# Kernel tuning notes

Measured on AMD Instinct MI355X. Metric: run time of the kernel, lower is better.

## Reference

```python
import jax, jax.numpy as jnp
import numpy as np

B, NV, NL, D, H = 32, 512, 256, 1024, 4096


def _ffn(x, w1, b1, w2, b2):
    # torch FFN: linear2(relu(linear1(x))); weights stored as [in, out]
    return jnp.maximum(x @ w1 + b1, 0.0) @ w2 + b2


def setup_inputs() -> dict:
    key = jax.random.key(0)
    ks = jax.random.split(key, 12)
    s_in = 1.0 / np.sqrt(D)
    s_h = 1.0 / np.sqrt(H)
    return {
        "V": jax.random.normal(ks[0], (B, NV, D), jnp.float32),
        "L": jax.random.normal(ks[1], (B, NL, D), jnp.float32),
        "v_mask": jnp.ones((B, NV), jnp.float32),
        "l_mask": jnp.ones((B, NL), jnp.float32),
        "w1_V": jax.random.normal(ks[2], (D, H), jnp.float32) * s_in,
        "b1_V": jnp.zeros((H,), jnp.float32),
        "w2_V": jax.random.normal(ks[3], (H, D), jnp.float32) * s_h,
        "b2_V": jnp.zeros((D,), jnp.float32),
        "w1_L": jax.random.normal(ks[4], (D, H), jnp.float32) * s_in,
        "b1_L": jnp.zeros((H,), jnp.float32),
        "w2_L": jax.random.normal(ks[5], (H, D), jnp.float32) * s_h,
        "b2_L": jnp.zeros((D,), jnp.float32),
    }


def reference(V, L, v_mask, l_mask, w1_V, b1_V, w2_V, b2_V, w1_L, b1_L, w2_L, b2_L):
    # masks are unused in the original forward
    fV_V = _ffn(V, w1_V, b1_V, w2_V, b2_V)  # [B, NV, D] = ffn_V(V)
    fL_L = _ffn(L, w1_L, b1_L, w2_L, b2_L)  # [B, NL, D] = ffn_L(L)
    fL_V = _ffn(V, w1_L, b1_L, w2_L, b2_L)  # [B, NV, D] = ffn_L(V) (as in source)
    scale = 1.0 / jnp.sqrt(jnp.asarray(V.shape[-1], V.dtype))
    A_LV = jnp.einsum('bnd,bmd->bnm', fV_V, fL_L) * scale  # [B, NV, NL]
    A_VV = jnp.einsum('bnd,bmd->bnm', fV_V, fL_V) * scale  # [B, NV, NV]
    A = jnp.concatenate([A_LV, A_VV], axis=-1)             # [B, NV, NL+NV]
    # softmax over dim=1 (rows), as in the source
    attn = jax.nn.softmax(A, axis=1)
    KV = jnp.concatenate([fL_L, fV_V], axis=1)              # [B, NL+NV, D]
    V_next = jnp.einsum('bnk,bkd->bnd', attn, KV)           # [B, NV, D]
    return (A, V_next)
```

## Files before the change

### kernel.cpp

```cpp
#include <hip/hip_runtime.h>
#include <stdint.h>

#define B_   32
#define NV_  512
#define NL_  256
#define D_   1024
#define H_   4096
#define KTOT 768
#define SCALE_ 0.03125f

typedef __attribute__((ext_vector_type(8))) __bf16 bf8_t;
typedef __attribute__((ext_vector_type(4))) float f32x4;

__device__ __forceinline__ unsigned short f2bf(float f) {
    unsigned u = __float_as_uint(f);
    u += 0x7FFFu + ((u >> 16) & 1u);
    return (unsigned short)(u >> 16);
}
__device__ __forceinline__ unsigned pk2(float lo, float hi) {
    return (unsigned)f2bf(lo) | ((unsigned)f2bf(hi) << 16);
}

__device__ __forceinline__ void gl_lds16(const void* g, const void* lds) {
    __builtin_amdgcn_global_load_lds(
        (const __attribute__((address_space(1))) unsigned int*)(uintptr_t)g,
        (__attribute__((address_space(3))) unsigned int*)(unsigned)(uintptr_t)lds,
        16, 0, 0);
}

#define SBAR() asm volatile("s_barrier" ::: "memory")
#define VMC4() asm volatile("s_waitcnt vmcnt(4)" ::: "memory")
#define VMC0() asm volatile("s_waitcnt vmcnt(0)" ::: "memory")

template<int EPI>
__global__ __launch_bounds__(512, 1)
void gemm256(const unsigned short* __restrict__ Ab, long sAz, int lda,
             const unsigned short* __restrict__ Bb, long sBz, int ldb,
             const float* __restrict__ bias,
             unsigned short* __restrict__ Cp, long sCz, int ldc, int K,
             int nx, int ntile, int tpc)
{
    extern __shared__ unsigned char lds[];
    unsigned char* const ldsA = lds;
    unsigned char* const ldsB = lds + 65536;

    const int tid = threadIdx.x;
    const int w = tid >> 6, l = tid & 63;
    const int wr = w >> 2, wc = w & 3;
    const int lrow = l & 15;
    const int kg = l >> 4;

    int t_, z;
    {
        const int bid = blockIdx.x;
        if (tpc > 0) { const int r = bid >> 3, c = bid & 7; z = r / tpc; t_ = c * tpc + r % tpc; }
        else         { z = bid / ntile; t_ = bid - z * ntile; }
    }
    const int n0 = (t_ % nx) * 256, m0 = (t_ / nx) * 256;

    const unsigned short* A  = Ab + (long)z * sAz;
    const unsigned short* Bg = Bb + (long)z * sBz;

    const int srow = tid >> 3;
    const int scol = ((tid & 7) * 8) ^ ((srow & 7) << 3);
    const int ntk = K >> 6;

    const int cs0 = (((l >> 4) * 16)) ^ ((l & 7) << 4);
    const int cs1 = (64 + ((l >> 4) * 16)) ^ ((l & 7) << 4);

    const unsigned short* const sp0 = Bg + (long)(n0 +   0 + srow) * ldb + scol;
    const unsigned short* const sp1 = Bg + (long)(n0 + 128 + srow) * ldb + scol;
    const unsigned short* const sp2 = A  + (long)(m0 +   0 + srow) * lda + scol;
    const unsigned short* const sp3 = A  + (long)(m0 + 128 + srow) * lda + scol;
    const long stB = (long)64 * ldb, stA = (long)64 * lda;

    f32x4 acc[8][4];
#pragma unroll
    for (int i = 0; i < 8; ++i)
#pragma unroll
        for (int j = 0; j < 4; ++j) acc[i][j] = (f32x4){0.f, 0.f, 0.f, 0.f};

#define STG(tau, part) do {                                                   \
        const int buf_ = (tau) & 1;                                           \
        const int kt_ = ((tau) < ntk ? (tau) : ntk - 1);                      \
        if ((part) < 2) {                                                     \
            const unsigned short* s_ = ((part) == 0 ? sp0 : sp1) + (long)kt_ * 64; \
            unsigned char* d_ = ldsB + (buf_ * 2 + (part)) * 16384 + w * 1024;\
            gl_lds16(s_, d_); gl_lds16(s_ + stB, d_ + 8192);                  \
        } else {                                                              \
            const unsigned short* s_ = ((part) == 2 ? sp2 : sp3) + (long)kt_ * 64; \
            unsigned char* d_ = ldsA + (buf_ * 2 + (part) - 2) * 16384 + w * 1024; \
            gl_lds16(s_, d_); gl_lds16(s_ + stA, d_ + 8192);                  \
        } } while (0)

    auto rdA = [&](int buf, int mf, int cs) -> bf8_t {
        return *(const bf8_t*)(ldsA + (buf * 2 + wr) * 16384 + (mf * 16 + lrow) * 128 + cs);
    };
    auto rdB = [&](int buf, int nf, int cs) -> bf8_t {
        return *(const bf8_t*)(ldsB + (buf * 2 + (wc >> 1)) * 16384 +
                               ((wc & 1) * 64 + nf * 16 + lrow) * 128 + cs);
    };

#define MQ(MO, NO, AREG, BREG)                                                \
    _Pragma("unroll")                                                         \
    for (int mf = 0; mf < 4; ++mf)                                            \
    _Pragma("unroll")                                                         \
        for (int nf = 0; nf < 2; ++nf) {                                      \
            acc[(MO)+mf][(NO)+nf] = __builtin_amdgcn_mfma_f32_16x16x32_bf16(  \
                AREG[mf][0], BREG[nf][0], acc[(MO)+mf][(NO)+nf], 0, 0, 0);    \
            acc[(MO)+mf][(NO)+nf] = __builtin_amdgcn_mfma_f32_16x16x32_bf16(  \
                AREG[mf][1], BREG[nf][1], acc[(MO)+mf][(NO)+nf], 0, 0, 0);    \
        }

    STG(0, 0); STG(0, 1); STG(0, 2); STG(0, 3);
    STG(1, 0); STG(1, 1);
    VMC4();
    SBAR();

    bf8_t a0[4][2], b0r[2][2], b1r[2][2];

#define TILE4(BUF, TAU)                                                       \
                      \
    _Pragma("unroll")                                                         \
    for (int mf = 0; mf < 4; ++mf) { a0[mf][0] = rdA(BUF, mf, cs0);           \
                                     a0[mf][1] = rdA(BUF, mf, cs1); }         \
    _Pragma("unroll")                                                         \
    for (int nf = 0; nf < 2; ++nf) { b0r[nf][0] = rdB(BUF, nf, cs0);          \
                                     b0r[nf][1] = rdB(BUF, nf, cs1); }        \
    STG((TAU) + 1, 2);                                                        \
    SBAR();                                                                   \
    __builtin_amdgcn_s_setprio(1);                                            \
    _Pragma("unroll")                                                         \
    for (int nf = 0; nf < 2; ++nf) { b1r[nf][0] = rdB(BUF, nf + 2, cs0);      \
                                     b1r[nf][1] = rdB(BUF, nf + 2, cs1); }    \
    MQ(0, 0, a0, b0r)                                                         \
    __builtin_amdgcn_s_setprio(0);                                            \
    SBAR();                                                                   \
                                                                      \
    STG((TAU) + 1, 3);                                                        \
    SBAR();                                                                   \
    __builtin_amdgcn_s_setprio(1);                                            \
    MQ(0, 2, a0, b1r)                                                         \
    __builtin_amdgcn_s_setprio(0);                                            \
    SBAR();                                                                   \
                           \
    _Pragma("unroll")                                                         \
    for (int mf = 0; mf < 4; ++mf) { a0[mf][0] = rdA(BUF, mf + 4, cs0);       \
                                     a0[mf][1] = rdA(BUF, mf + 4, cs1); }     \
    STG((TAU) + 2, 0);                                                        \
    SBAR();                                                                   \
    __builtin_amdgcn_s_setprio(1);                                            \
    MQ(4, 0, a0, b0r)                                                         \
    __builtin_amdgcn_s_setprio(0);                                            \
    SBAR();                                                                   \
                                                                      \
    STG((TAU) + 2, 1);                                                        \
    SBAR();                                                                   \
    VMC4();                                                                   \
    __builtin_amdgcn_s_setprio(1);                                            \
    MQ(4, 2, a0, b1r)                                                         \
    __builtin_amdgcn_s_setprio(0);                                            \
    SBAR();

    for (int t = 0; t < ntk; t += 2) {
        TILE4(0, t)
        TILE4(1, t + 1)
    }
#undef TILE4
#undef MQ
#undef STG

    VMC0();
    SBAR();

    unsigned short* C = Cp + (long)z * sCz;
    unsigned char* const scr = lds + w * 16384;

    float bv[4];
#pragma unroll
    for (int nf = 0; nf < 4; ++nf) bv[nf] = bias[n0 + wc * 64 + nf * 16 + lrow];

#pragma unroll
    for (int p = 0; p < 2; ++p) {
#pragma unroll
        for (int mf = 0; mf < 4; ++mf)
#pragma unroll
            for (int nf = 0; nf < 4; ++nf)
#pragma unroll
                for (int r = 0; r < 4; ++r) {
                    float v = acc[4 * p + mf][nf][r] + bv[nf];
                    if (EPI == 0) v = fmaxf(v, 0.f);
                    *(unsigned short*)(scr + (mf * 16 + kg * 4 + r) * 136 +
                                       (nf * 16 + lrow) * 2) = f2bf(v);
                }
#pragma unroll
        for (int it = 0; it < 8; ++it) {
            const int rr = it * 8 + (l >> 3);
            const uint4 q = *(const uint4*)(scr + rr * 136 + (l & 7) * 16);
            *(uint4*)(C + (long)(m0 + wr * 128 + p * 64 + rr) * ldc +
                      (n0 + wc * 64 + (l & 7) * 8)) = q;
        }
    }
}

__device__ __forceinline__ void supertile(int nx, int tpc, int& n0, int& m0, int& z)
{
    const int bid = blockIdx.x;
    const int r = bid >> 3, c = bid & 7;
    z = r / tpc;
    const int t = c * tpc + (r % tpc);
    n0 = (t % nx) * 128;
    m0 = (t / nx) * 128;
}

template<int EPI>
__global__ __launch_bounds__(256)
void mgemm(const unsigned short* __restrict__ Ab, long sAz, int lda,
           const unsigned short* __restrict__ Bb, long sBz, int ldb,
           const float* __restrict__ bias, float scale,
           void* __restrict__ Cp, long sCz, int ldc, int K,
           int nx, int tpc)
{
    __shared__ unsigned short As[128 * 32];
    __shared__ unsigned short Bs[128 * 32];

    const int tid = threadIdx.x;
    const int w = tid >> 6, l = tid & 63;
    const int wr = w >> 1, wc = w & 1;
    const int l15 = l & 15, kg = l >> 4;
    const int srow = l >> 2, scol = (l & 3) * 8;
    int n0, m0, z;
    supertile(nx, tpc, n0, m0, z);

    const unsigned short* A  = Ab + (long)z * sAz;
    const unsigned short* Bg = Bb + (long)z * sBz;

    f32x4 acc[4][4];
#pragma unroll
    for (int m = 0; m < 4; ++m)
#pragma unroll
        for (int n = 0; n < 4; ++n) acc[m][n] = (f32x4){0.f, 0.f, 0.f, 0.f};

    for (int k0 = 0; k0 < K; k0 += 32) {
#pragma unroll
        for (int i = 0; i < 2; ++i) {
            const int g = i * 4 + w;
            gl_lds16(A  + (long)(m0 + g * 16 + srow) * lda + (k0 + scol), &As[g * 512]);
            gl_lds16(Bg + (long)(n0 + g * 16 + srow) * ldb + (k0 + scol), &Bs[g * 512]);
        }
        __syncthreads();

        bf8_t af[4], bf[4];
#pragma unroll
        for (int m = 0; m < 4; ++m)
            af[m] = *(const bf8_t*)&As[(wr * 64 + m * 16 + l15) * 32 + kg * 8];
#pragma unroll
        for (int n = 0; n < 4; ++n)
            bf[n] = *(const bf8_t*)&Bs[(wc * 64 + n * 16 + l15) * 32 + kg * 8];
#pragma unroll
        for (int m = 0; m < 4; ++m)
#pragma unroll
            for (int n = 0; n < 4; ++n)
                acc[m][n] = __builtin_amdgcn_mfma_f32_16x16x32_bf16(af[m], bf[n], acc[m][n], 0, 0, 0);
        __syncthreads();
    }

    const int orow = wr * 64 + (l >> 4) * 4;
    const int ocol = wc * 64 + l15;
    if (EPI == 2) {
        float* C = (float*)Cp + (long)z * sCz;
#pragma unroll
        for (int m = 0; m < 4; ++m)
#pragma unroll
            for (int n = 0; n < 4; ++n)
#pragma unroll
                for (int r = 0; r < 4; ++r)
                    C[(long)(m0 + orow + m * 16 + r) * ldc + (n0 + ocol + n * 16)] =
                        acc[m][n][r] * scale;
    } else {
        unsigned short* C = (unsigned short*)Cp + (long)z * sCz;
#pragma unroll
        for (int n = 0; n < 4; ++n) {
            const float bvv = bias[n0 + ocol + n * 16];
#pragma unroll
            for (int m = 0; m < 4; ++m)
#pragma unroll
                for (int r = 0; r < 4; ++r) {
                    float v = acc[m][n][r] + bvv;
                    if (EPI == 0) v = fmaxf(v, 0.f);
                    C[(long)(m0 + orow + m * 16 + r) * ldc + (n0 + ocol + n * 16)] = f2bf(v);
                }
        }
    }
}

__global__ __launch_bounds__(256)
void col_stats(const float* __restrict__ A, float* __restrict__ Mst, float* __restrict__ RS)
{
    __shared__ float red[4][64];
    const int t = threadIdx.x;
    const int kk = t & 63, ng = t >> 6;
    const int k = blockIdx.x * 64 + kk;
    const int z = blockIdx.y;
    const float* base = A + (long)z * NV_ * KTOT + k;
    float m = -3.0e38f;
    for (int n = ng * 128; n < ng * 128 + 128; ++n) m = fmaxf(m, base[(long)n * KTOT]);
    red[ng][kk] = m;
    __syncthreads();
    m = fmaxf(fmaxf(red[0][kk], red[1][kk]), fmaxf(red[2][kk], red[3][kk]));
    float s = 0.f;
    for (int n = ng * 128; n < ng * 128 + 128; ++n) s += __expf(base[(long)n * KTOT] - m);
    __syncthreads();
    red[ng][kk] = s;
    __syncthreads();
    if (ng == 0) {
        s = red[0][kk] + red[1][kk] + red[2][kk] + red[3][kk];
        Mst[(long)z * KTOT + k] = m;
        RS[(long)z * KTOT + k]  = 1.f / s;
    }
}

__global__ __launch_bounds__(256)
void attn_mfma(const float* __restrict__ Ap, const unsigned short* __restrict__ KVt,
               const float* __restrict__ Mstp, const float* __restrict__ RSp,
               float* __restrict__ Cp, int nx, int tpc)
{
    __shared__ unsigned short As[128 * 32];
    __shared__ unsigned short Bs[128 * 32];

    const int tid = threadIdx.x;
    const int w = tid >> 6, l = tid & 63;
    const int wr = w >> 1, wc = w & 1;
    const int l15 = l & 15, kg = l >> 4;
    const int srow = l >> 2, scol = (l & 3) * 8;
    int n0, m0, z;
    supertile(nx, tpc, n0, m0, z);

    const float* A = Ap + (long)z * NV_ * KTOT;
    const unsigned short* Bg = KVt + (long)z * D_ * KTOT;
    const float* Mz = Mstp + (long)z * KTOT;
    const float* Rz = RSp  + (long)z * KTOT;
    float* C = Cp + (long)z * NV_ * D_;

    const int ar = tid >> 1;
    const int ah = (tid & 1) * 16;

    f32x4 acc[4][4];
#pragma unroll
    for (int m = 0; m < 4; ++m)
#pragma unroll
        for (int n = 0; n < 4; ++n) acc[m][n] = (f32x4){0.f, 0.f, 0.f, 0.f};

    for (int k0 = 0; k0 < KTOT; k0 += 32) {
#pragma unroll
        for (int i = 0; i < 2; ++i) {
            const int g = i * 4 + w;
            gl_lds16(Bg + (long)(n0 + g * 16 + srow) * KTOT + (k0 + scol), &Bs[g * 512]);
        }
        const float* arow = A + (long)(m0 + ar) * KTOT + k0 + ah;
        const float4 x0 = *(const float4*)(arow);
        const float4 x1 = *(const float4*)(arow + 4);
        const float4 x2 = *(const float4*)(arow + 8);
        const float4 x3 = *(const float4*)(arow + 12);
        const float4 ma = *(const float4*)(Mz + k0 + ah);
        const float4 mb = *(const float4*)(Mz + k0 + ah + 4);
        const float4 mc = *(const float4*)(Mz + k0 + ah + 8);
        const float4 md = *(const float4*)(Mz + k0 + ah + 12);
        const float4 ra = *(const float4*)(Rz + k0 + ah);
        const float4 rb = *(const float4*)(Rz + k0 + ah + 4);
        const float4 rc = *(const float4*)(Rz + k0 + ah + 8);
        const float4 rd = *(const float4*)(Rz + k0 + ah + 12);
        const unsigned q0 = pk2(__expf(x0.x - ma.x) * ra.x, __expf(x0.y - ma.y) * ra.y);
        const unsigned q1 = pk2(__expf(x0.z - ma.z) * ra.z, __expf(x0.w - ma.w) * ra.w);
        const unsigned q2 = pk2(__expf(x1.x - mb.x) * rb.x, __expf(x1.y - mb.y) * rb.y);
        const unsigned q3 = pk2(__expf(x1.z - mb.z) * rb.z, __expf(x1.w - mb.w) * rb.w);
        const unsigned q4 = pk2(__expf(x2.x - mc.x) * rc.x, __expf(x2.y - mc.y) * rc.y);
        const unsigned q5 = pk2(__expf(x2.z - mc.z) * rc.z, __expf(x2.w - mc.w) * rc.w);
        const unsigned q6 = pk2(__expf(x3.x - md.x) * rd.x, __expf(x3.y - md.y) * rd.y);
        const unsigned q7 = pk2(__expf(x3.z - md.z) * rd.z, __expf(x3.w - md.w) * rd.w);
        *(uint4*)&As[ar * 32 + ah]     = make_uint4(q0, q1, q2, q3);
        *(uint4*)&As[ar * 32 + ah + 8] = make_uint4(q4, q5, q6, q7);
        __syncthreads();

        bf8_t af[4], bf[4];
#pragma unroll
        for (int m = 0; m < 4; ++m)
            af[m] = *(const bf8_t*)&As[(wr * 64 + m * 16 + l15) * 32 + kg * 8];
#pragma unroll
        for (int n = 0; n < 4; ++n)
            bf[n] = *(const bf8_t*)&Bs[(wc * 64 + n * 16 + l15) * 32 + kg * 8];
#pragma unroll
        for (int m = 0; m < 4; ++m)
#pragma unroll
            for (int n = 0; n < 4; ++n)
                acc[m][n] = __builtin_amdgcn_mfma_f32_16x16x32_bf16(af[m], bf[n], acc[m][n], 0, 0, 0);
        __syncthreads();
    }

    const int orow = wr * 64 + (l >> 4) * 4;
    const int ocol = wc * 64 + l15;
#pragma unroll
    for (int m = 0; m < 4; ++m)
#pragma unroll
        for (int n = 0; n < 4; ++n)
#pragma unroll
            for (int r = 0; r < 4; ++r)
                C[(long)(m0 + orow + m * 16 + r) * D_ + (n0 + ocol + n * 16)] = acc[m][n][r];
}

__global__ __launch_bounds__(256)
void tr2bf_f(const float* __restrict__ src, long sSz, int ldS,
             unsigned short* __restrict__ dst, long sDz, int ldD)
{
    __shared__ unsigned short T[64][65];
    const int t = threadIdx.x;
    const int rr = t >> 2, cc = (t & 3) * 16;
    const int r0 = blockIdx.x * 64, c0 = blockIdx.y * 64, z = blockIdx.z;
    const float* S = src + (long)z * sSz + (long)(r0 + rr) * ldS + c0 + cc;
    const float4 a = *(const float4*)(S);
    const float4 b = *(const float4*)(S + 4);
    const float4 c = *(const float4*)(S + 8);
    const float4 d = *(const float4*)(S + 12);
    unsigned short* Tr = &T[rr][cc];
    Tr[0] = f2bf(a.x); Tr[1] = f2bf(a.y); Tr[2]  = f2bf(a.z); Tr[3]  = f2bf(a.w);
    Tr[4] = f2bf(b.x); Tr[5] = f2bf(b.y); Tr[6]  = f2bf(b.z); Tr[7]  = f2bf(b.w);
    Tr[8] = f2bf(c.x); Tr[9] = f2bf(c.y); Tr[10] = f2bf(c.z); Tr[11] = f2bf(c.w);
    Tr[12] = f2bf(d.x); Tr[13] = f2bf(d.y); Tr[14] = f2bf(d.z); Tr[15] = f2bf(d.w);
    __syncthreads();
    unsigned short v[16];
#pragma unroll
    for (int j = 0; j < 16; ++j) v[j] = T[cc + j][rr];
    unsigned q[8];
#pragma unroll
    for (int j = 0; j < 8; ++j) q[j] = (unsigned)v[2 * j] | ((unsigned)v[2 * j + 1] << 16);
    unsigned short* Dp = dst + (long)z * sDz + (long)(c0 + rr) * ldD + r0 + cc;
    *(uint4*)Dp       = make_uint4(q[0], q[1], q[2], q[3]);
    *(uint4*)(Dp + 8) = make_uint4(q[4], q[5], q[6], q[7]);
}

__global__ __launch_bounds__(256)
void tr2bf_h(const unsigned short* __restrict__ src, long sSz, int ldS,
             unsigned short* __restrict__ dst, long sDz, int ldD)
{
    __shared__ unsigned short T[64][65];
    const int t = threadIdx.x;
    const int rr = t >> 2, cc = (t & 3) * 16;
    const int r0 = blockIdx.x * 64, c0 = blockIdx.y * 64, z = blockIdx.z;
    const unsigned short* S = src + (long)z * sSz + (long)(r0 + rr) * ldS + c0 + cc;
    const uint4 qa = *(const uint4*)(S);
    const uint4 qb = *(const uint4*)(S + 8);
    unsigned short* Tr = &T[rr][cc];
    Tr[0]  = qa.x & 0xFFFF; Tr[1]  = qa.x >> 16; Tr[2]  = qa.y & 0xFFFF; Tr[3]  = qa.y >> 16;
    Tr[4]  = qa.z & 0xFFFF; Tr[5]  = qa.z >> 16; Tr[6]  = qa.w & 0xFFFF; Tr[7]  = qa.w >> 16;
    Tr[8]  = qb.x & 0xFFFF; Tr[9]  = qb.x >> 16; Tr[10] = qb.y & 0xFFFF; Tr[11] = qb.y >> 16;
    Tr[12] = qb.z & 0xFFFF; Tr[13] = qb.z >> 16; Tr[14] = qb.w & 0xFFFF; Tr[15] = qb.w >> 16;
    __syncthreads();
    unsigned short v[16];
#pragma unroll
    for (int j = 0; j < 16; ++j) v[j] = T[cc + j][rr];
    unsigned q[8];
#pragma unroll
    for (int j = 0; j < 8; ++j) q[j] = (unsigned)v[2 * j] | ((unsigned)v[2 * j + 1] << 16);
    unsigned short* Dp = dst + (long)z * sDz + (long)(c0 + rr) * ldD + r0 + cc;
    *(uint4*)Dp       = make_uint4(q[0], q[1], q[2], q[3]);
    *(uint4*)(Dp + 8) = make_uint4(q[4], q[5], q[6], q[7]);
}

__global__ __launch_bounds__(256)
void cvt_bf(const float* __restrict__ src, unsigned short* __restrict__ dst, long n)
{
    const long i = ((long)blockIdx.x * 256 + threadIdx.x) * 8;
    if (i >= n) return;
    const float4 a = *(const float4*)(src + i);
    const float4 b = *(const float4*)(src + i + 4);
    *(uint4*)(dst + i) = make_uint4(pk2(a.x, a.y), pk2(a.z, a.w), pk2(b.x, b.y), pk2(b.z, b.w));
}

extern "C" void kernel_launch(void* const* d_in, const int* in_sizes, int n_in,
                              void* d_out, int out_size, void* d_ws, size_t ws_size,
                              hipStream_t stream)
{
    (void)in_sizes; (void)n_in; (void)out_size;

    const float* V   = (const float*)d_in[0];
    const float* L   = (const float*)d_in[1];
    const float* w1V = (const float*)d_in[4];
    const float* b1V = (const float*)d_in[5];
    const float* w2V = (const float*)d_in[6];
    const float* b2V = (const float*)d_in[7];
    const float* w1L = (const float*)d_in[8];
    const float* b1L = (const float*)d_in[9];
    const float* w2L = (const float*)d_in[10];
    const float* b2L = (const float*)d_in[11];

    float* outA = (float*)d_out;
    float* outV = outA + (size_t)B_ * NV_ * KTOT;

    unsigned short* w1Vt = (unsigned short*)d_ws;
    unsigned short* w2Vt = w1Vt + (size_t)H_ * D_;
    unsigned short* w1Lt = w2Vt + (size_t)D_ * H_;
    unsigned short* w2Lt = w1Lt + (size_t)H_ * D_;
    unsigned short* pool = w2Lt + (size_t)D_ * H_;

    const size_t perb_us = (size_t)NV_ * D_ + (size_t)NL_ * D_ + (size_t)NV_ * H_ +
                           (size_t)NV_ * D_ + (size_t)NL_ * D_ + (size_t)NV_ * D_ +
                           (size_t)D_ * KTOT;
    const size_t perb_bytes = perb_us * 2 + 2 * (size_t)KTOT * sizeof(float);
    const size_t persist_bytes = (size_t)4 * H_ * D_ * 2;
    const size_t avail = (ws_size > persist_bytes + 256) ? ws_size - persist_bytes - 256 : 0;
    int bc = (int)(avail / perb_bytes);
    if (bc > B_) bc = B_;
    if (bc < 1)  bc = 1;

    unsigned short* Vb  = pool;
    unsigned short* Lb  = Vb  + (size_t)bc * NV_ * D_;
    unsigned short* hid = Lb  + (size_t)bc * NL_ * D_;
    unsigned short* fV  = hid + (size_t)bc * NV_ * H_;
    unsigned short* fLL = fV  + (size_t)bc * NV_ * D_;
    unsigned short* fLV = fLL + (size_t)bc * NL_ * D_;
    unsigned short* KVt = fLV + (size_t)bc * NV_ * D_;
    float* Mst = (float*)(KVt + (size_t)bc * D_ * KTOT);
    float* RS  = Mst + (size_t)bc * KTOT;

    const dim3 blk(256);
    const dim3 blk5(512);

    {
        auto* f0 = gemm256<0>;
        auto* f1 = gemm256<1>;
        hipFuncSetAttribute((const void*)f0, hipFuncAttributeMaxDynamicSharedMemorySize, 131072);
        hipFuncSetAttribute((const void*)f1, hipFuncAttributeMaxDynamicSharedMemorySize, 131072);
    }

    tr2bf_f<<<dim3(D_ / 64, H_ / 64, 1), blk, 0, stream>>>(w1V, 0, H_, w1Vt, 0, D_);
    tr2bf_f<<<dim3(H_ / 64, D_ / 64, 1), blk, 0, stream>>>(w2V, 0, D_, w2Vt, 0, H_);
    tr2bf_f<<<dim3(D_ / 64, H_ / 64, 1), blk, 0, stream>>>(w1L, 0, H_, w1Lt, 0, D_);
    tr2bf_f<<<dim3(H_ / 64, D_ / 64, 1), blk, 0, stream>>>(w2L, 0, D_, w2Lt, 0, H_);

    for (int b0 = 0; b0 < B_; b0 += bc) {
        const int cur = (B_ - b0 < bc) ? (B_ - b0) : bc;

        cvt_bf<<<dim3(cur * NV_ * D_ / 2048), blk, 0, stream>>>(
            V + (size_t)b0 * NV_ * D_, Vb, (long)cur * NV_ * D_);
        cvt_bf<<<dim3(cur * NL_ * D_ / 2048), blk, 0, stream>>>(
            L + (size_t)b0 * NL_ * D_, Lb, (long)cur * NL_ * D_);

        #define G256(M, N) dim3((unsigned)(((N) / 256) * ((M) / 256) * cur)), blk5, 131072, stream
        #define P256(M, N) (N) / 256, (((N) / 256) * ((M) / 256)), \
                           ((((N) / 256) * ((M) / 256)) % 8 == 0 ? (((N) / 256) * ((M) / 256)) / 8 : 0)

        gemm256<0><<<G256(NV_, H_)>>>(Vb, (long)NV_ * D_, D_, w1Vt, 0, D_, b1V,
                                      hid, (long)NV_ * H_, H_, D_, P256(NV_, H_));
        gemm256<1><<<G256(NV_, D_)>>>(hid, (long)NV_ * H_, H_, w2Vt, 0, H_, b2V,
                                      fV, (long)NV_ * D_, D_, H_, P256(NV_, D_));
        gemm256<0><<<G256(NL_, H_)>>>(Lb, (long)NL_ * D_, D_, w1Lt, 0, D_, b1L,
                                      hid, (long)NV_ * H_, H_, D_, P256(NL_, H_));
        gemm256<1><<<G256(NL_, D_)>>>(hid, (long)NV_ * H_, H_, w2Lt, 0, H_, b2L,
                                      fLL, (long)NL_ * D_, D_, H_, P256(NL_, D_));
        gemm256<0><<<G256(NV_, H_)>>>(Vb, (long)NV_ * D_, D_, w1Lt, 0, D_, b1L,
                                      hid, (long)NV_ * H_, H_, D_, P256(NV_, H_));
        gemm256<1><<<G256(NV_, D_)>>>(hid, (long)NV_ * H_, H_, w2Lt, 0, H_, b2L,
                                      fLV, (long)NV_ * D_, D_, H_, P256(NV_, D_));
        #undef G256
        #undef P256

        #define GRID(nx, ny) dim3((unsigned)((nx) * (ny) * cur)), blk
        #define SWZ(nx, ny)  (nx), ((nx) * (ny) / 8)
        mgemm<2><<<GRID(NL_ / 128, NV_ / 128), 0, stream>>>(
            fV, (long)NV_ * D_, D_, fLL, (long)NL_ * D_, D_, nullptr, SCALE_,
            outA + (size_t)b0 * NV_ * KTOT, (long)NV_ * KTOT, KTOT, D_,
            SWZ(NL_ / 128, NV_ / 128));
        mgemm<2><<<GRID(NV_ / 128, NV_ / 128), 0, stream>>>(
            fV, (long)NV_ * D_, D_, fLV, (long)NV_ * D_, D_, nullptr, SCALE_,
            outA + (size_t)b0 * NV_ * KTOT + NL_, (long)NV_ * KTOT, KTOT, D_,
            SWZ(NV_ / 128, NV_ / 128));

        tr2bf_h<<<dim3(NL_ / 64, D_ / 64, cur), blk, 0, stream>>>(
            fLL, (long)NL_ * D_, D_, KVt, (long)D_ * KTOT, KTOT);
        tr2bf_h<<<dim3(NV_ / 64, D_ / 64, cur), blk, 0, stream>>>(
            fV, (long)NV_ * D_, D_, KVt + NL_, (long)D_ * KTOT, KTOT);

        col_stats<<<dim3(KTOT / 64, cur), blk, 0, stream>>>(
            outA + (size_t)b0 * NV_ * KTOT, Mst, RS);

        attn_mfma<<<GRID(D_ / 128, NV_ / 128), 0, stream>>>(
            outA + (size_t)b0 * NV_ * KTOT, KVt, Mst, RS,
            outV + (size_t)b0 * NV_ * D_, SWZ(D_ / 128, NV_ / 128));
        #undef GRID
        #undef SWZ
    }
}
```

Baseline: 937.1 us.

## Restructure GEMM main loop into two phases with cross-tile register prefetch

Reworks the inner K-loop of the bf16 MFMA GEMM from four barrier-separated quarter phases into two halves per tile. Fragments for the next tile's first half are read from the other LDS buffer during the second half of the current tile, using double-buffered register sets. This cuts the number of workgroup barriers and overlaps LDS reads with MFMA issue. In exchange it raises VGPR use (three fragment sets are live), which may lower occupancy, and it relies on the reordered staging and vmcnt waits keeping the LDS buffers hazard-free.

```diff
diff --git a/kernel.cpp b/kernel.cpp
--- a/kernel.cpp
+++ b/kernel.cpp
@@ -117,56 +117,50 @@
     VMC4();
     SBAR();
 
-    bf8_t a0[4][2], b0r[2][2], b1r[2][2];
-
-#define TILE4(BUF, TAU)                                                       \
-                      \
+    bf8_t a0A[4][2], b0A[2][2];
+    bf8_t a0B[4][2], b0B[2][2];
+    bf8_t a1r[4][2], b1r[2][2];
+
+#pragma unroll
+    for (int mf = 0; mf < 4; ++mf) { a0A[mf][0] = rdA(0, mf, cs0);
+                                     a0A[mf][1] = rdA(0, mf, cs1); }
+#pragma unroll
+    for (int nf = 0; nf < 2; ++nf) { b0A[nf][0] = rdB(0, nf, cs0);
+                                     b0A[nf][1] = rdB(0, nf, cs1); }
+
+#define TILEX(BUF, A0C, B0C, A0N, B0N, TAU)                                   \
+    STG((TAU) + 1, 2); STG((TAU) + 1, 3);                                     \
+    __builtin_amdgcn_s_setprio(1);                                            \
     _Pragma("unroll")                                                         \
-    for (int mf = 0; mf < 4; ++mf) { a0[mf][0] = rdA(BUF, mf, cs0);           \
-                                     a0[mf][1] = rdA(BUF, mf, cs1); }         \
-    _Pragma("unroll")                                                         \
-    for (int nf = 0; nf < 2; ++nf) { b0r[nf][0] = rdB(BUF, nf, cs0);          \
-                                     b0r[nf][1] = rdB(BUF, nf, cs1); }        \
-    STG((TAU) + 1, 2);                                                        \
-    SBAR();                                                                   \
-    __builtin_amdgcn_s_setprio(1);                                            \
+    for (int mf = 0; mf < 4; ++mf) { a1r[mf][0] = rdA(BUF, mf + 4, cs0);      \
+                                     a1r[mf][1] = rdA(BUF, mf + 4, cs1); }    \
     _Pragma("unroll")                                                         \
     for (int nf = 0; nf < 2; ++nf) { b1r[nf][0] = rdB(BUF, nf + 2, cs0);      \
                                      b1r[nf][1] = rdB(BUF, nf + 2, cs1); }    \
-    MQ(0, 0, a0, b0r)                                                         \
+    MQ(0, 0, A0C, B0C)                                                        \
+    MQ(0, 2, A0C, b1r)                                                        \
     __builtin_amdgcn_s_setprio(0);                                            \
-    SBAR();                                                                   \
-                                                                      \
-    STG((TAU) + 1, 3);                                                        \
-    SBAR();                                                                   \
+    SBAR();                                            \
+    STG((TAU) + 2, 0); STG((TAU) + 2, 1);                                     \
+    VMC4();                                                                   \
+    SBAR();                                       \
     __builtin_amdgcn_s_setprio(1);                                            \
-    MQ(0, 2, a0, b1r)                                                         \
-    __builtin_amdgcn_s_setprio(0);                                            \
-    SBAR();                                                                   \
-                           \
     _Pragma("unroll")                                                         \
-    for (int mf = 0; mf < 4; ++mf) { a0[mf][0] = rdA(BUF, mf + 4, cs0);       \
-                                     a0[mf][1] = rdA(BUF, mf + 4, cs1); }     \
-    STG((TAU) + 2, 0);                                                        \
-    SBAR();                                                                   \
-    __builtin_amdgcn_s_setprio(1);                                            \
-    MQ(4, 0, a0, b0r)                                                         \
-    __builtin_amdgcn_s_setprio(0);                                            \
-    SBAR();                                                                   \
-                                                                      \
-    STG((TAU) + 2, 1);                                                        \
-    SBAR();                                                                   \
-    VMC4();                                                                   \
-    __builtin_amdgcn_s_setprio(1);                                            \
-    MQ(4, 2, a0, b1r)                                                         \
+    for (int mf = 0; mf < 4; ++mf) { A0N[mf][0] = rdA((BUF) ^ 1, mf, cs0);    \
+                                     A0N[mf][1] = rdA((BUF) ^ 1, mf, cs1); }  \
+    _Pragma("unroll")                                                         \
+    for (int nf = 0; nf < 2; ++nf) { B0N[nf][0] = rdB((BUF) ^ 1, nf, cs0);    \
+                                     B0N[nf][1] = rdB((BUF) ^ 1, nf, cs1); }  \
+    MQ(4, 0, a1r, B0C)                                                        \
+    MQ(4, 2, a1r, b1r)                                                        \
     __builtin_amdgcn_s_setprio(0);                                            \
     SBAR();
 
     for (int t = 0; t < ntk; t += 2) {
-        TILE4(0, t)
-        TILE4(1, t + 1)
-    }
-#undef TILE4
+        TILEX(0, a0A, b0A, a0B, b0B, t)
+        TILEX(1, a0B, b0B, a0A, b0A, t + 1)
+    }
+#undef TILEX
 #undef MQ
 #undef STG
 
```

Result: no change. 929.7 us (-0.8%).
